# Optimization experiments

Hardware: AMD Instinct MI355X
Metric: run time of the kernel (lower is better)

The kernel has to match this reference:

```python
import jax, jax.numpy as jnp
import numpy as np

NUM_HEADS = 8
HIDDEN_DIM = 256
QUERY_DIM = 256
HEAD_DIM = HIDDEN_DIM // NUM_HEADS
NORM_FACT = float(HIDDEN_DIM / NUM_HEADS) ** (-0.5)


def setup_inputs() -> dict:
    key = jax.random.key(0)
    k1, k2, k3, k4, k5 = jax.random.split(key, 5)
    B, Q, H, W = 16, 100, 64, 64
    q = jax.random.normal(k1, (B, Q, QUERY_DIM), dtype=jnp.float32)
    k = jax.random.normal(k2, (B, QUERY_DIM, H, W), dtype=jnp.float32)
    mask = jax.random.randint(k3, (B, H, W), 0, 2).astype(jnp.bool_)
    # xavier_uniform for [hidden, query] linear weights
    limit = float(np.sqrt(6.0 / (HIDDEN_DIM + QUERY_DIM)))
    Wq = jax.random.uniform(k4, (HIDDEN_DIM, QUERY_DIM), minval=-limit, maxval=limit, dtype=jnp.float32)
    Wk = jax.random.uniform(k5, (HIDDEN_DIM, QUERY_DIM), minval=-limit, maxval=limit, dtype=jnp.float32)
    bq = jnp.zeros((HIDDEN_DIM,), dtype=jnp.float32)
    bk = jnp.zeros((HIDDEN_DIM,), dtype=jnp.float32)
    return {"q": q, "k": k, "Wq": Wq, "bq": bq, "Wk": Wk, "bk": bk, "mask": mask}


def reference(q, k, Wq, bq, Wk, bk, mask):
    B, Q, _ = q.shape
    _, C, H, W = k.shape
    # q projection: [B, Q, hidden]
    qp = jnp.einsum('bqc,hc->bqh', q, Wq) + bq
    # k projection via 1x1 conv == channelwise linear: [B, hidden, H, W]
    kp = jnp.einsum('bchw,oc->bohw', k, Wk) + bk[None, :, None, None]
    # split heads: qh [B,Q,nh,hd], kh [B,nh,hd,H,W]
    qh = qp.reshape(B, Q, NUM_HEADS, HEAD_DIM)
    kh = kp.reshape(B, NUM_HEADS, HEAD_DIM, H, W)
    # scores [B,Q,nh,H,W]
    weights = jnp.einsum('bqnd,bndhw->bqnhw', qh, kh) * NORM_FACT
    # masked fill: mask [B,H,W] -> broadcast over (Q, heads)
    weights = jnp.where(mask[:, None, None, :, :], -jnp.inf, weights)
    # softmax jointly over (heads, H, W), as in torch flatten(2)
    flat = weights.reshape(B, Q, NUM_HEADS * H * W)
    flat = jax.nn.softmax(flat, axis=-1)
    return flat.reshape(B, Q, NUM_HEADS, H, W)
```

## Files before the change

### kernel.cpp

```cpp
#include <hip/hip_runtime.h>
#include <hip/hip_bf16.h>
#include <math.h>

#define BB 16
#define QQ 100
#define NH 8
#define HD 32
#define HWN 4096
#define NORM_FACT 0.17677669529663687f
#define QPAD 112

typedef short bf16x8_t __attribute__((ext_vector_type(8)));
typedef float f32x4_t  __attribute__((ext_vector_type(4)));

__device__ __forceinline__ unsigned short bf16bits(float f) {
    __hip_bfloat16 h = __float2bfloat16(f);
    return __builtin_bit_cast(unsigned short, h);
}
__device__ __forceinline__ float bf16tof(unsigned short u) {
    union { unsigned int i; float f; } x; x.i = (unsigned int)u << 16; return x.f;
}

__global__ void k_prep(const float* __restrict__ Wq, const float* __restrict__ Wk,
                       float* __restrict__ WqT, unsigned short* __restrict__ Wkbf) {
    int idx = blockIdx.x;
    int h = threadIdx.x;
    if (idx < 256) {
        WqT[idx * 256 + h] = Wq[h * 256 + idx];
    } else {
        int r = idx - 256;
        Wkbf[r * 256 + h] = bf16bits(Wk[r * 256 + h]);
    }
}

__global__ __launch_bounds__(256) void k_qproj(const float* __restrict__ q,
                                               const float* __restrict__ WqT,
                                               const float* __restrict__ bq,
                                               unsigned short* __restrict__ qphi,
                                               unsigned short* __restrict__ qplo) {
    int blk = blockIdx.x;
    int b = blk / 28, q0 = (blk % 28) * 4;
    int h = threadIdx.x;
    size_t obase = ((size_t)b * QPAD + q0) * 256 + h;
    if (q0 >= QQ) {
#pragma unroll
        for (int i = 0; i < 4; ++i) { qphi[obase + i * 256] = 0; qplo[obase + i * 256] = 0; }
        return;
    }
    __shared__ float qsh[4][256];
    int ibase = (b * QQ + q0) * 256;
#pragma unroll
    for (int i = 0; i < 4; ++i) qsh[i][h] = q[ibase + i * 256 + h];
    __syncthreads();
    float bias = bq[h];
    float a0 = bias, a1 = bias, a2 = bias, a3 = bias;
    for (int c = 0; c < 256; ++c) {
        float wv = WqT[c * 256 + h];
        a0 = fmaf(qsh[0][c], wv, a0);
        a1 = fmaf(qsh[1][c], wv, a1);
        a2 = fmaf(qsh[2][c], wv, a2);
        a3 = fmaf(qsh[3][c], wv, a3);
    }
    float a[4] = {a0 * NORM_FACT, a1 * NORM_FACT, a2 * NORM_FACT, a3 * NORM_FACT};
#pragma unroll
    for (int i = 0; i < 4; ++i) {
        unsigned short hi = bf16bits(a[i]);
        qphi[obase + i * 256] = hi;
        qplo[obase + i * 256] = bf16bits(a[i] - bf16tof(hi));
    }
}

__global__ __launch_bounds__(256) void k_tconv(const float* __restrict__ k,
                                               unsigned short* __restrict__ kT) {
    int b = blockIdx.z, c0 = blockIdx.y * 64, hw0 = blockIdx.x * 64;
    int t = threadIdx.x;
    __shared__ float lds[64][65];
    const float* src = k + ((size_t)b * 256 + c0) * HWN + hw0;
    int col = t & 63, r0 = t >> 6;
#pragma unroll
    for (int i = 0; i < 16; ++i) {
        int r = i * 4 + r0;
        lds[r][col] = src[(size_t)r * HWN + col];
    }
    __syncthreads();
    int hw = t >> 2, cc = (t & 3) * 16;
    unsigned short* dst = kT + ((size_t)b * HWN + hw0 + hw) * 256 + c0 + cc;
    uint4 v0, v1;
    unsigned int* w0 = (unsigned int*)&v0;
    unsigned int* w1 = (unsigned int*)&v1;
#pragma unroll
    for (int j = 0; j < 4; ++j) {
        w0[j] = (unsigned int)bf16bits(lds[cc + 2*j + 0][hw])
              | ((unsigned int)bf16bits(lds[cc + 2*j + 1][hw]) << 16);
        w1[j] = (unsigned int)bf16bits(lds[cc + 8 + 2*j + 0][hw])
              | ((unsigned int)bf16bits(lds[cc + 8 + 2*j + 1][hw]) << 16);
    }
    *(uint4*)(dst)     = v0;
    *(uint4*)(dst + 8) = v1;
}

__global__ __launch_bounds__(256) void k_fused(const unsigned short* __restrict__ kT,
                                               const unsigned short* __restrict__ Wkbf,
                                               const float* __restrict__ bk,
                                               const unsigned short* __restrict__ qphi,
                                               const unsigned short* __restrict__ qplo,
                                               const int* __restrict__ mask,
                                               unsigned short* __restrict__ kpT,
                                               float* __restrict__ partial) {
    int b = blockIdx.y;
    int hwblk = blockIdx.x * 64;
    int t = threadIdx.x;
    int w = t >> 6, lane = t & 63;
    int n15 = lane & 15;
    int kg = lane >> 4;
    int hw = hwblk + w * 16 + n15;

    f32x4_t acc[16];
#pragma unroll
    for (int m = 0; m < 16; ++m) acc[m] = f32x4_t{0.f, 0.f, 0.f, 0.f};

    const unsigned short* kTrow = kT + ((size_t)b * HWN + hw) * 256 + kg * 8;
    const unsigned short* wbase = Wkbf + (size_t)n15 * 256 + kg * 8;

#pragma unroll 2
    for (int ks = 0; ks < 8; ++ks) {
        bf16x8_t bfrag = *reinterpret_cast<const bf16x8_t*>(kTrow + ks * 32);
#pragma unroll
        for (int m = 0; m < 16; ++m) {
            bf16x8_t afrag = *reinterpret_cast<const bf16x8_t*>(wbase + (size_t)m * 16 * 256 + ks * 32);
            acc[m] = __builtin_amdgcn_mfma_f32_16x16x32_bf16(afrag, bfrag, acc[m], 0, 0, 0);
        }
    }

    __shared__ unsigned short tile2[64 * 264];
    int hw_l = w * 16 + n15;
#pragma unroll
    for (int m = 0; m < 16; ++m) {
        ushort4 pk;
        unsigned short* pkp = (unsigned short*)&pk;
#pragma unroll
        for (int r = 0; r < 4; ++r) {
            int o = m * 16 + kg * 4 + r;
            pkp[r] = bf16bits(acc[m][r] + bk[o]);
        }
        *(ushort4*)&tile2[hw_l * 264 + m * 16 + kg * 4] = pk;
    }
    __syncthreads();

    int hw_r = t >> 2, sub = t & 3;
    unsigned short* dst = kpT + ((size_t)b * HWN + hwblk + hw_r) * 256;
#pragma unroll
    for (int j = 0; j < 8; ++j) {
        int o = j * 32 + sub * 8;
        uint4 v = *(uint4*)&tile2[hw_r * 264 + o];
        *(uint4*)(dst + o) = v;
    }

    float mm = mask[b * HWN + hw] ? 0.0f : 1.0f;
    const unsigned short* ahi_b = qphi + ((size_t)(b * QPAD + n15)) * 256 + kg * 8;
    const unsigned short* alo_b = qplo + ((size_t)(b * QPAD + n15)) * 256 + kg * 8;
    float sums[7][4] = {};
#pragma unroll 1
    for (int n = 0; n < NH; ++n) {
        bf16x8_t bfr = *reinterpret_cast<const bf16x8_t*>(&tile2[hw_l * 264 + n * 32 + kg * 8]);
#pragma unroll
        for (int mt = 0; mt < 7; ++mt) {
            bf16x8_t ahi = *reinterpret_cast<const bf16x8_t*>(ahi_b + (size_t)(mt * 16) * 256 + n * 32);
            bf16x8_t alo = *reinterpret_cast<const bf16x8_t*>(alo_b + (size_t)(mt * 16) * 256 + n * 32);
            f32x4_t a2 = {0.f, 0.f, 0.f, 0.f};
            a2 = __builtin_amdgcn_mfma_f32_16x16x32_bf16(ahi, bfr, a2, 0, 0, 0);
            a2 = __builtin_amdgcn_mfma_f32_16x16x32_bf16(alo, bfr, a2, 0, 0, 0);
#pragma unroll
            for (int r = 0; r < 4; ++r)
                sums[mt][r] += __expf(a2[r]) * mm;
        }
    }
#pragma unroll
    for (int mt = 0; mt < 7; ++mt)
#pragma unroll
        for (int r = 0; r < 4; ++r) {
            float v = sums[mt][r];
            v += __shfl_xor(v, 1, 64);
            v += __shfl_xor(v, 2, 64);
            v += __shfl_xor(v, 4, 64);
            v += __shfl_xor(v, 8, 64);
            if (n15 == 0) {
                int qrow = mt * 16 + kg * 4 + r;
                partial[((size_t)b * QPAD + qrow) * 256 + blockIdx.x * 4 + w] = v;
            }
        }
}

__global__ __launch_bounds__(256) void k_invsum(const float* __restrict__ partial,
                                                float* __restrict__ inv) {
    int blk = blockIdx.x;
    int b = blk / QQ, qq = blk % QQ;
    const float* p = partial + ((size_t)b * QPAD + qq) * 256;
    int t = threadIdx.x;
    float v = p[t];
#pragma unroll
    for (int off = 32; off; off >>= 1) v += __shfl_xor(v, off, 64);
    __shared__ float red[4];
    if ((t & 63) == 0) red[t >> 6] = v;
    __syncthreads();
    if (t == 0) inv[blk] = 1.0f / (red[0] + red[1] + red[2] + red[3]);
}

__global__ __launch_bounds__(256) void k_write(const unsigned short* __restrict__ qphi,
                                               const unsigned short* __restrict__ qplo,
                                               const unsigned short* __restrict__ kpT,
                                               const int* __restrict__ mask,
                                               const float* __restrict__ inv,
                                               float* __restrict__ out) {
    int hws = blockIdx.x, qt = blockIdx.y, b = blockIdx.z;
    int t = threadIdx.x, w = t >> 6, lane = t & 63;
    int n15 = lane & 15, kg = lane >> 4;
    int hw0 = hws * 256 + w * 64;
    float mm[4];
#pragma unroll
    for (int ht = 0; ht < 4; ++ht)
        mm[ht] = mask[b * HWN + hw0 + ht * 16 + n15] ? 0.0f : 1.0f;
    float invq[4];
#pragma unroll
    for (int r = 0; r < 4; ++r) {
        int qrow = qt * 16 + kg * 4 + r;
        invq[r] = (qrow < QQ) ? inv[b * QQ + qrow] : 0.0f;
    }
    const unsigned short* ahi_b = qphi + ((size_t)(b * QPAD + qt * 16 + n15)) * 256 + kg * 8;
    const unsigned short* alo_b = qplo + ((size_t)(b * QPAD + qt * 16 + n15)) * 256 + kg * 8;
    const unsigned short* brow  = kpT  + ((size_t)(b * HWN + hw0 + n15)) * 256 + kg * 8;
    __shared__ float lt[4][16][65];
#pragma unroll 1
    for (int n = 0; n < NH; ++n) {
        bf16x8_t bf[4];
#pragma unroll
        for (int ht = 0; ht < 4; ++ht)
            bf[ht] = *reinterpret_cast<const bf16x8_t*>(brow + (size_t)(ht * 16) * 256 + n * 32);
        bf16x8_t ahi = *reinterpret_cast<const bf16x8_t*>(ahi_b + n * 32);
        bf16x8_t alo = *reinterpret_cast<const bf16x8_t*>(alo_b + n * 32);
#pragma unroll
        for (int ht = 0; ht < 4; ++ht) {
            f32x4_t acc = {0.f, 0.f, 0.f, 0.f};
            acc = __builtin_amdgcn_mfma_f32_16x16x32_bf16(ahi, bf[ht], acc, 0, 0, 0);
            acc = __builtin_amdgcn_mfma_f32_16x16x32_bf16(alo, bf[ht], acc, 0, 0, 0);
#pragma unroll
            for (int r = 0; r < 4; ++r)
                lt[w][kg * 4 + r][ht * 16 + n15] = __expf(acc[r]) * mm[ht] * invq[r];
        }
        __syncthreads();
#pragma unroll
        for (int rr = 0; rr < 16; ++rr) {
            int qrow = qt * 16 + rr;
            if (qrow < QQ)
                out[(((size_t)(b * QQ + qrow)) * NH + n) * HWN + hw0 + lane] = lt[w][rr][lane];
        }
        __syncthreads();
    }
}

extern "C" void kernel_launch(void* const* d_in, const int* in_sizes, int n_in,
                              void* d_out, int out_size, void* d_ws, size_t ws_size,
                              hipStream_t stream) {
    const float* q    = (const float*)d_in[0];
    const float* k    = (const float*)d_in[1];
    const float* Wq   = (const float*)d_in[2];
    const float* bq   = (const float*)d_in[3];
    const float* Wk   = (const float*)d_in[4];
    const float* bk   = (const float*)d_in[5];
    const int*   mask = (const int*)d_in[6];
    float* out = (float*)d_out;

    char* base = (char*)d_ws;
    unsigned short* kT   = (unsigned short*)(base);
    unsigned short* kpT  = (unsigned short*)(base + 33554432);
    unsigned short* qphi = (unsigned short*)(base + 67108864);
    unsigned short* qplo = (unsigned short*)(base + 68026368);
    float*  WqT     = (float*)(base + 68943872);
    unsigned short* Wkbf = (unsigned short*)(base + 69206016);
    float*  partial = (float*)(base + 69337088);
    float*  inv     = (float*)(base + 71172096);
    if (ws_size < (size_t)71178496) return;

    k_prep  <<<dim3(512), dim3(256), 0, stream>>>(Wq, Wk, WqT, Wkbf);
    k_qproj <<<dim3(448), dim3(256), 0, stream>>>(q, WqT, bq, qphi, qplo);
    k_tconv <<<dim3(64, 4, 16), dim3(256), 0, stream>>>(k, kT);
    k_fused <<<dim3(64, 16), dim3(256), 0, stream>>>(kT, Wkbf, bk, qphi, qplo, mask, kpT, partial);
    k_invsum<<<dim3(1600), dim3(256), 0, stream>>>(partial, inv);
    k_write <<<dim3(16, 7, 16), dim3(256), 0, stream>>>(qphi, qplo, kpT, mask, inv, out);
}
```

Before: 233.1 us.

## Split fused kproj/sums kernel and vectorize nontemporal output stores

Splits the fused projection+sum kernel into a k-projection kernel with twice as many blocks (each computing half the output channels) and a separate sums kernel that reads kpT from global memory and preloads q fragments. The final write kernel drops its block barriers, since each wave uses its own LDS slice, and stores float4 values with nontemporal hints. The aim is more parallelism and cheaper streaming of the large output. The cost is an extra launch and an extra global read of kpT.

New measurement: 223.0 us. -4.3%, faster.

```diff
diff --git a/kernel.cpp b/kernel.cpp
--- a/kernel.cpp
+++ b/kernel.cpp
@@ -99,77 +99,87 @@
     *(uint4*)(dst + 8) = v1;
 }
 
-__global__ __launch_bounds__(256) void k_fused(const unsigned short* __restrict__ kT,
+__global__ __launch_bounds__(256) void k_kproj(const unsigned short* __restrict__ kT,
                                                const unsigned short* __restrict__ Wkbf,
                                                const float* __restrict__ bk,
-                                               const unsigned short* __restrict__ qphi,
-                                               const unsigned short* __restrict__ qplo,
-                                               const int* __restrict__ mask,
-                                               unsigned short* __restrict__ kpT,
-                                               float* __restrict__ partial) {
+                                               unsigned short* __restrict__ kpT) {
     int b = blockIdx.y;
-    int hwblk = blockIdx.x * 64;
+    int hwblk = blockIdx.x * 32;
     int t = threadIdx.x;
     int w = t >> 6, lane = t & 63;
+    int hwt = w & 1, oh = w >> 1;
     int n15 = lane & 15;
     int kg = lane >> 4;
-    int hw = hwblk + w * 16 + n15;
-
-    f32x4_t acc[16];
-#pragma unroll
-    for (int m = 0; m < 16; ++m) acc[m] = f32x4_t{0.f, 0.f, 0.f, 0.f};
+    int hw = hwblk + hwt * 16 + n15;
+
+    f32x4_t acc[8];
+#pragma unroll
+    for (int m = 0; m < 8; ++m) acc[m] = f32x4_t{0.f, 0.f, 0.f, 0.f};
 
     const unsigned short* kTrow = kT + ((size_t)b * HWN + hw) * 256 + kg * 8;
-    const unsigned short* wbase = Wkbf + (size_t)n15 * 256 + kg * 8;
+    const unsigned short* wbase = Wkbf + ((size_t)(oh * 128 + n15)) * 256 + kg * 8;
 
 #pragma unroll 2
     for (int ks = 0; ks < 8; ++ks) {
         bf16x8_t bfrag = *reinterpret_cast<const bf16x8_t*>(kTrow + ks * 32);
 #pragma unroll
-        for (int m = 0; m < 16; ++m) {
+        for (int m = 0; m < 8; ++m) {
             bf16x8_t afrag = *reinterpret_cast<const bf16x8_t*>(wbase + (size_t)m * 16 * 256 + ks * 32);
             acc[m] = __builtin_amdgcn_mfma_f32_16x16x32_bf16(afrag, bfrag, acc[m], 0, 0, 0);
         }
     }
 
-    __shared__ unsigned short tile2[64 * 264];
-    int hw_l = w * 16 + n15;
-#pragma unroll
-    for (int m = 0; m < 16; ++m) {
+    __shared__ unsigned short tile2[32 * 264];
+    int hw_l = hwt * 16 + n15;
+#pragma unroll
+    for (int m = 0; m < 8; ++m) {
         ushort4 pk;
         unsigned short* pkp = (unsigned short*)&pk;
 #pragma unroll
         for (int r = 0; r < 4; ++r) {
-            int o = m * 16 + kg * 4 + r;
+            int o = oh * 128 + m * 16 + kg * 4 + r;
             pkp[r] = bf16bits(acc[m][r] + bk[o]);
         }
-        *(ushort4*)&tile2[hw_l * 264 + m * 16 + kg * 4] = pk;
+        *(ushort4*)&tile2[hw_l * 264 + oh * 128 + m * 16 + kg * 4] = pk;
     }
     __syncthreads();
-
-    int hw_r = t >> 2, sub = t & 3;
-    unsigned short* dst = kpT + ((size_t)b * HWN + hwblk + hw_r) * 256;
-#pragma unroll
-    for (int j = 0; j < 8; ++j) {
-        int o = j * 32 + sub * 8;
-        uint4 v = *(uint4*)&tile2[hw_r * 264 + o];
-        *(uint4*)(dst + o) = v;
-    }
-
+    int row = t >> 3, sub = t & 7;
+    unsigned short* dst = kpT + ((size_t)b * HWN + hwblk + row) * 256 + sub * 32;
+    const unsigned short* srcl = &tile2[row * 264 + sub * 32];
+#pragma unroll
+    for (int j = 0; j < 4; ++j)
+        *(uint4*)(dst + j * 8) = *(const uint4*)(srcl + j * 8);
+}
+
+__global__ __launch_bounds__(256) void k_sums(const unsigned short* __restrict__ qphi,
+                                              const unsigned short* __restrict__ qplo,
+                                              const unsigned short* __restrict__ kpT,
+                                              const int* __restrict__ mask,
+                                              float* __restrict__ partial) {
+    int b = blockIdx.y;
+    int hwblk = blockIdx.x * 64;
+    int t = threadIdx.x, w = t >> 6, lane = t & 63;
+    int n15 = lane & 15, kg = lane >> 4;
+    int hw = hwblk + w * 16 + n15;
     float mm = mask[b * HWN + hw] ? 0.0f : 1.0f;
+    const unsigned short* brow  = kpT  + ((size_t)(b * HWN + hw)) * 256 + kg * 8;
     const unsigned short* ahi_b = qphi + ((size_t)(b * QPAD + n15)) * 256 + kg * 8;
     const unsigned short* alo_b = qplo + ((size_t)(b * QPAD + n15)) * 256 + kg * 8;
     float sums[7][4] = {};
 #pragma unroll 1
     for (int n = 0; n < NH; ++n) {
-        bf16x8_t bfr = *reinterpret_cast<const bf16x8_t*>(&tile2[hw_l * 264 + n * 32 + kg * 8]);
+        bf16x8_t ahi[7], alo[7];
 #pragma unroll
         for (int mt = 0; mt < 7; ++mt) {
-            bf16x8_t ahi = *reinterpret_cast<const bf16x8_t*>(ahi_b + (size_t)(mt * 16) * 256 + n * 32);
-            bf16x8_t alo = *reinterpret_cast<const bf16x8_t*>(alo_b + (size_t)(mt * 16) * 256 + n * 32);
+            ahi[mt] = *reinterpret_cast<const bf16x8_t*>(ahi_b + (size_t)(mt * 16) * 256 + n * 32);
+            alo[mt] = *reinterpret_cast<const bf16x8_t*>(alo_b + (size_t)(mt * 16) * 256 + n * 32);
+        }
+        bf16x8_t bfr = *reinterpret_cast<const bf16x8_t*>(brow + n * 32);
+#pragma unroll
+        for (int mt = 0; mt < 7; ++mt) {
             f32x4_t a2 = {0.f, 0.f, 0.f, 0.f};
-            a2 = __builtin_amdgcn_mfma_f32_16x16x32_bf16(ahi, bfr, a2, 0, 0, 0);
-            a2 = __builtin_amdgcn_mfma_f32_16x16x32_bf16(alo, bfr, a2, 0, 0, 0);
+            a2 = __builtin_amdgcn_mfma_f32_16x16x32_bf16(ahi[mt], bfr, a2, 0, 0, 0);
+            a2 = __builtin_amdgcn_mfma_f32_16x16x32_bf16(alo[mt], bfr, a2, 0, 0, 0);
 #pragma unroll
             for (int r = 0; r < 4; ++r)
                 sums[mt][r] += __expf(a2[r]) * mm;
@@ -229,7 +239,7 @@
     const unsigned short* ahi_b = qphi + ((size_t)(b * QPAD + qt * 16 + n15)) * 256 + kg * 8;
     const unsigned short* alo_b = qplo + ((size_t)(b * QPAD + qt * 16 + n15)) * 256 + kg * 8;
     const unsigned short* brow  = kpT  + ((size_t)(b * HWN + hw0 + n15)) * 256 + kg * 8;
-    __shared__ float lt[4][16][65];
+    __shared__ float lt[4][16][68];
 #pragma unroll 1
     for (int n = 0; n < NH; ++n) {
         bf16x8_t bf[4];
@@ -247,14 +257,15 @@
             for (int r = 0; r < 4; ++r)
                 lt[w][kg * 4 + r][ht * 16 + n15] = __expf(acc[r]) * mm[ht] * invq[r];
         }
-        __syncthreads();
-#pragma unroll
-        for (int rr = 0; rr < 16; ++rr) {
+#pragma unroll
+        for (int j = 0; j < 4; ++j) {
+            int rr = j * 4 + kg;
             int qrow = qt * 16 + rr;
+            f32x4_t v4 = *(const f32x4_t*)&lt[w][rr][n15 * 4];
             if (qrow < QQ)
-                out[(((size_t)(b * QQ + qrow)) * NH + n) * HWN + hw0 + lane] = lt[w][rr][lane];
-        }
-        __syncthreads();
+                __builtin_nontemporal_store(v4,
+                    (f32x4_t*)(out + (((size_t)(b * QQ + qrow)) * NH + n) * HWN + hw0 + n15 * 4));
+        }
     }
 }
 
@@ -284,7 +295,8 @@
     k_prep  <<<dim3(512), dim3(256), 0, stream>>>(Wq, Wk, WqT, Wkbf);
     k_qproj <<<dim3(448), dim3(256), 0, stream>>>(q, WqT, bq, qphi, qplo);
     k_tconv <<<dim3(64, 4, 16), dim3(256), 0, stream>>>(k, kT);
-    k_fused <<<dim3(64, 16), dim3(256), 0, stream>>>(kT, Wkbf, bk, qphi, qplo, mask, kpT, partial);
+    k_kproj <<<dim3(128, 16), dim3(256), 0, stream>>>(kT, Wkbf, bk, kpT);
+    k_sums  <<<dim3(64, 16), dim3(256), 0, stream>>>(qphi, qplo, kpT, mask, partial);
     k_invsum<<<dim3(1600), dim3(256), 0, stream>>>(partial, inv);
     k_write <<<dim3(16, 7, 16), dim3(256), 0, stream>>>(qphi, qplo, kpT, mask, inv, out);
 }
```
